# Performance work log

Hardware: AMD Instinct MI355X
Metric: run time of the kernel (lower is better)

## Reference

```python
import jax, jax.numpy as jnp
import numpy as np

B, S, DIM = 4, 2048, 2048
H, KVH, HD = 32, 8, 64
REPEATS = H // KVH
SCALE = HD ** -0.5


def _rope(x, cos, sin):
    # x: (B, S, Hn, HD); cos/sin: (S, HD//2)
    xr = x[..., 0::2]
    xi = x[..., 1::2]
    c = cos[:, None, :]  # (S, 1, HD//2) broadcasts over heads
    s = sin[:, None, :]
    out_r = xr * c - xi * s
    out_i = xr * s + xi * c
    return jnp.stack([out_r, out_i], axis=-1).reshape(x.shape)


def setup_inputs() -> dict:
    key = jax.random.key(0)
    ks = jax.random.split(key, 5)
    x = jax.random.normal(ks[0], (B, S, DIM), dtype=jnp.float32)
    wq = jax.random.normal(ks[1], (H * HD, DIM), dtype=jnp.float32) * 0.02
    wk = jax.random.normal(ks[2], (KVH * HD, DIM), dtype=jnp.float32) * 0.02
    wv = jax.random.normal(ks[3], (KVH * HD, DIM), dtype=jnp.float32) * 0.02
    wo = jax.random.normal(ks[4], (DIM, H * HD), dtype=jnp.float32) * 0.02
    # standard RoPE frequencies: freqs_cis = exp(i * t * theta)
    inv_freq = 1.0 / (10000.0 ** (jnp.arange(0, HD, 2, dtype=jnp.float32) / HD))
    angles = jnp.arange(S, dtype=jnp.float32)[:, None] * inv_freq[None, :]  # (S, HD//2)
    return {
        "x": x, "wq": wq, "wk": wk, "wv": wv, "wo": wo,
        "freqs_cos": jnp.cos(angles), "freqs_sin": jnp.sin(angles),
    }


def reference(x, wq, wk, wv, wo, freqs_cos, freqs_sin):
    b, s, _ = x.shape
    q = (x @ wq.T).reshape(b, s, H, HD)
    k = (x @ wk.T).reshape(b, s, KVH, HD)
    v = (x @ wv.T).reshape(b, s, KVH, HD)
    q = _rope(q, freqs_cos, freqs_sin)
    k = _rope(k, freqs_cos, freqs_sin)
    k_rep = jnp.repeat(k, REPEATS, axis=2)  # (B,S,H,HD)
    v_rep = jnp.repeat(v, REPEATS, axis=2)
    # NOTE: faithful to source - q is NOT transposed to (B,H,S,HD), so the
    # matmul contracts head_dim at each token, producing (B,S,H,H) scores
    # (mixing across heads per position), softmaxed over the last head axis.
    scores = jnp.einsum('bshd,bsed->bshe', q, k_rep) * SCALE  # (B,S,H,H)
    weights = jax.nn.softmax(scores, axis=-1)
    out = jnp.einsum('bshe,bsed->bshd', weights, v_rep)  # (B,S,H,HD)
    out = out.reshape(b, s, H * HD)
    return out @ wo.T
```

## Files before the change

kernel.cpp:

```cpp
#include <hip/hip_runtime.h>

typedef unsigned short u16;
typedef __bf16 bf16x8 __attribute__((ext_vector_type(8)));
typedef float f32x4 __attribute__((ext_vector_type(4)));

#define AS1 __attribute__((address_space(1)))
#define AS3 __attribute__((address_space(3)))

__device__ inline u16 f2bf(float f) {
    union { float f; unsigned u; } c; c.f = f;
    unsigned u = c.u;
    u += 0x7fffu + ((u >> 16) & 1u);
    return (u16)(u >> 16);
}
__device__ inline float bf2f(u16 b) {
    union { unsigned u; float f; } c; c.u = ((unsigned)b) << 16;
    return c.f;
}

__device__ inline void async_cp16(const void* g, void* l) {
    __builtin_amdgcn_global_load_lds((const AS1 void*)g, (AS3 void*)l, 16, 0, 0);
}

__global__ __launch_bounds__(256)
void f32_to_bf16_x8(const float* __restrict__ src, u16* __restrict__ dst) {
    int i = (blockIdx.x * 256 + threadIdx.x) * 8;
    float4 f0 = *(const float4*)(src + i);
    float4 f1 = *(const float4*)(src + i + 4);
    union { u16 h[8]; uint4 v; } o;
    o.h[0] = f2bf(f0.x); o.h[1] = f2bf(f0.y);
    o.h[2] = f2bf(f0.z); o.h[3] = f2bf(f0.w);
    o.h[4] = f2bf(f1.x); o.h[5] = f2bf(f1.y);
    o.h[6] = f2bf(f1.z); o.h[7] = f2bf(f1.w);
    *(uint4*)(dst + i) = o.v;
}

__global__ __launch_bounds__(256)
void conv_weights(const float* __restrict__ wq, const float* __restrict__ wk,
                  const float* __restrict__ wv, const float* __restrict__ wo,
                  u16* __restrict__ wqkv, u16* __restrict__ wo_bf) {
    int i = (blockIdx.x * 256 + threadIdx.x) * 4;
    const float* src;
    u16* dst;
    if (i < 4194304)       { src = wq + i;           dst = wqkv + i; }
    else if (i < 5242880)  { src = wk + (i-4194304); dst = wqkv + i; }
    else if (i < 6291456)  { src = wv + (i-5242880); dst = wqkv + i; }
    else                   { src = wo + (i-6291456); dst = wo_bf + (i-6291456); }
    float4 f = *(const float4*)src;
    union { u16 h[4]; uint2 v; } o;
    o.h[0] = f2bf(f.x); o.h[1] = f2bf(f.y);
    o.h[2] = f2bf(f.z); o.h[3] = f2bf(f.w);
    *(uint2*)dst = o.v;
}

template <bool BF16_OUT>
__global__ __launch_bounds__(256)
void gemm_bt(const u16* __restrict__ A, const u16* __restrict__ B,
             void* __restrict__ Cout, int N, int K) {
    __shared__ u16 ldsA[128 * 64];
    __shared__ u16 ldsB[128 * 64];

    const int tid  = threadIdx.x;
    const int wave = tid >> 6;
    const int lane = tid & 63;
    const int row0 = blockIdx.x * 128;
    const int col0 = blockIdx.y * 128;
    const int waveM = (wave >> 1) * 64;
    const int waveN = (wave & 1) * 64;
    const int lm   = lane & 15;
    const int quad = lane >> 4;

    const int sr  = lane >> 3;
    const int stR = 8 * wave + sr;
    const int stC = ((lane & 7) ^ sr) * 8;
    const u16* gA = A + (size_t)(row0 + stR) * K + stC;
    const u16* gB = B + (size_t)(col0 + stR) * K + stC;
    char* lA = (char*)ldsA + wave * 1024;
    char* lB = (char*)ldsB + wave * 1024;
    const size_t g32K = (size_t)32 * K;

    f32x4 acc[4][4];
#pragma unroll
    for (int i = 0; i < 4; i++)
#pragma unroll
        for (int j = 0; j < 4; j++) acc[i][j] = (f32x4){0.f, 0.f, 0.f, 0.f};

    int aOff[2][4], bOff[2][4];
#pragma unroll
    for (int s = 0; s < 2; s++)
#pragma unroll
        for (int mi = 0; mi < 4; mi++) {
            int rA = waveM + mi * 16 + lm;
            int rB = waveN + mi * 16 + lm;
            int c  = (4 * s + quad) ^ (lm & 7);
            aOff[s][mi] = rA * 128 + c * 16;
            bOff[s][mi] = rB * 128 + c * 16;
        }

    for (int kb = 0; kb < K; kb += 64) {
#pragma unroll
        for (int i = 0; i < 4; i++)
            async_cp16(gA + i * g32K + kb, lA + i * 4096);
#pragma unroll
        for (int i = 0; i < 4; i++)
            async_cp16(gB + i * g32K + kb, lB + i * 4096);
        __syncthreads();

#pragma unroll
        for (int s = 0; s < 2; s++) {
            bf16x8 af[4], bg[4];
#pragma unroll
            for (int mi = 0; mi < 4; mi++)
                af[mi] = *(const bf16x8*)((const char*)ldsA + aOff[s][mi]);
#pragma unroll
            for (int ni = 0; ni < 4; ni++)
                bg[ni] = *(const bf16x8*)((const char*)ldsB + bOff[s][ni]);
#pragma unroll
            for (int mi = 0; mi < 4; mi++)
#pragma unroll
                for (int ni = 0; ni < 4; ni++)
                    acc[mi][ni] = __builtin_amdgcn_mfma_f32_16x16x32_bf16(
                        af[mi], bg[ni], acc[mi][ni], 0, 0, 0);
        }
        __syncthreads();
    }

    const int rbase = row0 + waveM + quad * 4;
    const int cbase = col0 + waveN + lm;
    if (BF16_OUT) {
        u16* C = (u16*)Cout;
#pragma unroll
        for (int mi = 0; mi < 4; mi++)
#pragma unroll
            for (int r = 0; r < 4; r++) {
                size_t ro = (size_t)(rbase + mi * 16 + r) * N;
#pragma unroll
                for (int ni = 0; ni < 4; ni++)
                    C[ro + cbase + ni * 16] = f2bf(acc[mi][ni][r]);
            }
    } else {
        float* C = (float*)Cout;
#pragma unroll
        for (int mi = 0; mi < 4; mi++)
#pragma unroll
            for (int r = 0; r < 4; r++) {
                size_t ro = (size_t)(rbase + mi * 16 + r) * N;
#pragma unroll
                for (int ni = 0; ni < 4; ni++)
                    C[ro + cbase + ni * 16] = acc[mi][ni][r];
            }
    }
}

__global__ __launch_bounds__(256)
void attn_tok(const u16* __restrict__ qkv, u16* __restrict__ out) {
    __shared__ float kvf[1024];
    const int tok = blockIdx.x;
    const int t = threadIdx.x;
    const u16* qrow = qkv + (size_t)tok * 3072;

    {
        uint2 w = *(const uint2*)(qrow + 2048 + t * 4);
        kvf[t * 4 + 0] = bf2f((u16)(w.x & 0xffff));
        kvf[t * 4 + 1] = bf2f((u16)(w.x >> 16));
        kvf[t * 4 + 2] = bf2f((u16)(w.y & 0xffff));
        kvf[t * 4 + 3] = bf2f((u16)(w.y >> 16));
    }
    __syncthreads();

    const int h = t >> 3, j = t & 7;
    float qf[8];
    {
        uint4 w = *(const uint4*)(qrow + h * 64 + j * 8);
        unsigned ws4[4] = {w.x, w.y, w.z, w.w};
#pragma unroll
        for (int i = 0; i < 4; i++) {
            qf[2 * i]     = bf2f((u16)(ws4[i] & 0xffff));
            qf[2 * i + 1] = bf2f((u16)(ws4[i] >> 16));
        }
    }

    float s[8];
#pragma unroll
    for (int g = 0; g < 8; g++) {
        const float* kk = kvf + g * 64 + j * 8;
        float a = 0.f;
#pragma unroll
        for (int d = 0; d < 8; d++) a += qf[d] * kk[d];
        s[g] = a;
    }
#pragma unroll
    for (int g = 0; g < 8; g++) {
        s[g] += __shfl_xor(s[g], 1);
        s[g] += __shfl_xor(s[g], 2);
        s[g] += __shfl_xor(s[g], 4);
    }
    float m = -1e30f;
#pragma unroll
    for (int g = 0; g < 8; g++) { s[g] *= 0.125f; m = fmaxf(m, s[g]); }
    float p[8], l = 0.f;
#pragma unroll
    for (int g = 0; g < 8; g++) { p[g] = __expf(s[g] - m); l += p[g]; }
    float rl = 1.f / l;

    float o[8] = {0, 0, 0, 0, 0, 0, 0, 0};
#pragma unroll
    for (int g = 0; g < 8; g++) {
        float w = p[g] * rl;
        const float* vv = kvf + 512 + g * 64 + j * 8;
#pragma unroll
        for (int d = 0; d < 8; d++) o[d] += w * vv[d];
    }

    unsigned po[4];
#pragma unroll
    for (int i = 0; i < 4; i++)
        po[i] = (unsigned)f2bf(o[2 * i]) | ((unsigned)f2bf(o[2 * i + 1]) << 16);
    uint4 wo_; wo_.x = po[0]; wo_.y = po[1]; wo_.z = po[2]; wo_.w = po[3];
    *(uint4*)(out + (size_t)tok * 2048 + h * 64 + j * 8) = wo_;
}

extern "C" void kernel_launch(void* const* d_in, const int* in_sizes, int n_in,
                              void* d_out, int out_size, void* d_ws, size_t ws_size,
                              hipStream_t stream) {
    const float* x  = (const float*)d_in[0];
    const float* wq = (const float*)d_in[1];
    const float* wk = (const float*)d_in[2];
    const float* wv = (const float*)d_in[3];
    const float* wo = (const float*)d_in[4];

    u16* x_bf  = (u16*)d_ws;
    u16* wqkv  = x_bf  + 16777216;
    u16* wo_bf = wqkv  + 6291456;
    u16* qkv   = wo_bf + 4194304;
    u16* attn  = qkv   + 25165824;

    dim3 blk(256);
    f32_to_bf16_x8<<<8192, blk, 0, stream>>>(x, x_bf);
    conv_weights<<<10240, blk, 0, stream>>>(wq, wk, wv, wo, wqkv, wo_bf);

    gemm_bt<true><<<dim3(64, 24), blk, 0, stream>>>(x_bf, wqkv, qkv, 3072, 2048);

    attn_tok<<<8192, blk, 0, stream>>>(qkv, attn);

    gemm_bt<false><<<dim3(64, 16), blk, 0, stream>>>(attn, wo_bf, (float*)d_out,
                                                     2048, 2048);
}
```

Before: 376.0 us.

## Replace GEMM with 256x256-tile, 8-wave, double-buffered async-LDS pipelined kernel

Both projection GEMMs now use a new kernel with 256x256 output tiles per 512-thread block. It double-buffers 64-wide K slices in 128KB of LDS and issues async global-to-LDS copies for the next slices while MFMAs run on the current ones. Manual waitcnt, barrier and setprio scheduling interleave LDS fragment reads with MFMA phases. This is meant to hide global-load latency and raise data reuse per LDS byte. In exchange it launches far fewer blocks (384 and 256), so it depends on one wave of large blocks keeping all CUs busy, and it adds heavy register pressure.

```diff
diff --git a/kernel.cpp b/kernel.cpp
--- a/kernel.cpp
+++ b/kernel.cpp
@@ -54,83 +54,140 @@
 }
 
 template <bool BF16_OUT>
-__global__ __launch_bounds__(256)
-void gemm_bt(const u16* __restrict__ A, const u16* __restrict__ B,
-             void* __restrict__ Cout, int N, int K) {
-    __shared__ u16 ldsA[128 * 64];
-    __shared__ u16 ldsB[128 * 64];
+__global__ __launch_bounds__(512, 2)
+void gemm_bt8(const u16* __restrict__ A, const u16* __restrict__ B,
+              void* __restrict__ Cout, int N, int K) {
+    __shared__ __align__(16) u16 lds[65536];
+    char* ldsc = (char*)lds;
 
     const int tid  = threadIdx.x;
-    const int wave = tid >> 6;
+    const int w    = tid >> 6;
     const int lane = tid & 63;
-    const int row0 = blockIdx.x * 128;
-    const int col0 = blockIdx.y * 128;
-    const int waveM = (wave >> 1) * 64;
-    const int waveN = (wave & 1) * 64;
-    const int lm   = lane & 15;
-    const int quad = lane >> 4;
+    const int row0 = blockIdx.x * 256;
+    const int col0 = blockIdx.y * 256;
+    const int wm = w >> 2, wn = w & 3;
+    const int lm = lane & 15, quad = lane >> 4;
+
+    const int NT  = K / 64;
+    const int NIT = K / 128;
+    const int K64 = K * 64, K128 = K * 128;
 
     const int sr  = lane >> 3;
-    const int stR = 8 * wave + sr;
     const int stC = ((lane & 7) ^ sr) * 8;
-    const u16* gA = A + (size_t)(row0 + stR) * K + stC;
-    const u16* gB = B + (size_t)(col0 + stR) * K + stC;
-    char* lA = (char*)ldsA + wave * 1024;
-    char* lB = (char*)ldsB + wave * 1024;
-    const size_t g32K = (size_t)32 * K;
-
-    f32x4 acc[4][4];
-#pragma unroll
-    for (int i = 0; i < 4; i++)
+    const u16* pA = A + (size_t)(row0 + w * 8 + sr) * K + stC;
+    const u16* pB = B + (size_t)(col0 + w * 8 + sr) * K + stC;
+    const int stagoff = w * 1024;
+
+    const int cx0   = (quad ^ (lm & 7)) * 16;
+    const int cx1   = cx0 ^ 64;
+    const int aBase = (wm * 128 + lm) * 128;
+    const int bBase = 32768 + (wn * 64 + lm) * 128;
+
+    f32x4 acc[8][4];
+#pragma unroll
+    for (int i = 0; i < 8; i++)
 #pragma unroll
         for (int j = 0; j < 4; j++) acc[i][j] = (f32x4){0.f, 0.f, 0.f, 0.f};
 
-    int aOff[2][4], bOff[2][4];
-#pragma unroll
-    for (int s = 0; s < 2; s++)
-#pragma unroll
-        for (int mi = 0; mi < 4; mi++) {
-            int rA = waveM + mi * 16 + lm;
-            int rB = waveN + mi * 16 + lm;
-            int c  = (4 * s + quad) ^ (lm & 7);
-            aOff[s][mi] = rA * 128 + c * 16;
-            bOff[s][mi] = rB * 128 + c * 16;
-        }
-
-    for (int kb = 0; kb < K; kb += 64) {
-#pragma unroll
-        for (int i = 0; i < 4; i++)
-            async_cp16(gA + i * g32K + kb, lA + i * 4096);
-#pragma unroll
-        for (int i = 0; i < 4; i++)
-            async_cp16(gB + i * g32K + kb, lB + i * 4096);
-        __syncthreads();
-
-#pragma unroll
-        for (int s = 0; s < 2; s++) {
-            bf16x8 af[4], bg[4];
-#pragma unroll
-            for (int mi = 0; mi < 4; mi++)
-                af[mi] = *(const bf16x8*)((const char*)ldsA + aOff[s][mi]);
-#pragma unroll
-            for (int ni = 0; ni < 4; ni++)
-                bg[ni] = *(const bf16x8*)((const char*)ldsB + bOff[s][ni]);
-#pragma unroll
-            for (int mi = 0; mi < 4; mi++)
-#pragma unroll
-                for (int ni = 0; ni < 4; ni++)
-                    acc[mi][ni] = __builtin_amdgcn_mfma_f32_16x16x32_bf16(
-                        af[mi], bg[ni], acc[mi][ni], 0, 0, 0);
-        }
-        __syncthreads();
-    }
-
-    const int rbase = row0 + waveM + quad * 4;
-    const int cbase = col0 + waveN + lm;
+    auto stA = [&](int v, int h) {
+        int kb = (v < NT ? v : NT - 1) * 64;
+        const u16* g = pA + h * K128 + kb;
+        char* d = ldsc + ((v & 1) << 16) + h * 16384 + stagoff;
+        async_cp16(g, d);
+        async_cp16(g + K64, d + 8192);
+    };
+    auto stB = [&](int v, int h) {
+        int kb = (v < NT ? v : NT - 1) * 64;
+        const u16* g = pB + h * K128 + kb;
+        char* d = ldsc + ((v & 1) << 16) + 32768 + h * 16384 + stagoff;
+        async_cp16(g, d);
+        async_cp16(g + K64, d + 8192);
+    };
+
+    stB(0, 0); stB(0, 1); stA(0, 0); stA(0, 1);
+    stB(1, 0); stB(1, 1); stA(1, 0);
+    asm volatile("s_waitcnt vmcnt(6)" ::: "memory");
+    __builtin_amdgcn_s_barrier();
+
+    bf16x8 bg[4][2], afX[2][2], afY[2][2];
+
+#define LDR(off) (*(const bf16x8*)(ldsc + (off)))
+
+#define PHASE_TAIL(MI0, AF)                                                   \
+    __builtin_amdgcn_s_barrier();                                             \
+    asm volatile("s_waitcnt lgkmcnt(0)" ::: "memory");                        \
+    __builtin_amdgcn_sched_barrier(0);                                        \
+    __builtin_amdgcn_s_setprio(1);                                            \
+    _Pragma("unroll")                                                         \
+    for (int s = 0; s < 2; s++)                                               \
+        _Pragma("unroll")                                                     \
+        for (int j = 0; j < 2; j++)                                           \
+            _Pragma("unroll")                                                 \
+            for (int ni = 0; ni < 4; ni++)                                    \
+                acc[(MI0) + j][ni] = __builtin_amdgcn_mfma_f32_16x16x32_bf16( \
+                    AF[j][s], bg[ni][s], acc[(MI0) + j][ni], 0, 0, 0);        \
+    __builtin_amdgcn_s_setprio(0);
+
+#define HALF_ITER(u, BO)                                                      \
+    {                                                                         \
+                                                                      \
+        _Pragma("unroll")                                                     \
+        for (int ni = 0; ni < 4; ni++) {                                      \
+            bg[ni][0] = LDR((BO) + bBase + ni * 2048 + cx0);                  \
+            bg[ni][1] = LDR((BO) + bBase + ni * 2048 + cx1);                  \
+        }                                                                     \
+        _Pragma("unroll")                                                     \
+        for (int j = 0; j < 2; j++) {                                         \
+            afX[j][0] = LDR((BO) + aBase + j * 2048 + cx0);                   \
+            afX[j][1] = LDR((BO) + aBase + j * 2048 + cx1);                   \
+            afY[j][0] = LDR((BO) + aBase + (2 + j) * 2048 + cx0);             \
+            afY[j][1] = LDR((BO) + aBase + (2 + j) * 2048 + cx1);             \
+        }                                                                     \
+        stA((u) + 1, 1);                                                      \
+        asm volatile("s_waitcnt lgkmcnt(8)" ::: "memory");                    \
+        PHASE_TAIL(0, afX)                                                    \
+        __builtin_amdgcn_s_barrier();                                         \
+                                                                      \
+        _Pragma("unroll")                                                     \
+        for (int j = 0; j < 2; j++) {                                         \
+            afX[j][0] = LDR((BO) + aBase + (4 + j) * 2048 + cx0);             \
+            afX[j][1] = LDR((BO) + aBase + (4 + j) * 2048 + cx1);             \
+        }                                                                     \
+        stB((u) + 2, 0);                                                      \
+        PHASE_TAIL(2, afY)                                                    \
+        __builtin_amdgcn_s_barrier();                                         \
+                                                                      \
+        _Pragma("unroll")                                                     \
+        for (int j = 0; j < 2; j++) {                                         \
+            afY[j][0] = LDR((BO) + aBase + (6 + j) * 2048 + cx0);             \
+            afY[j][1] = LDR((BO) + aBase + (6 + j) * 2048 + cx1);             \
+        }                                                                     \
+        stB((u) + 2, 1);                                                      \
+        PHASE_TAIL(4, afX)                                                    \
+        __builtin_amdgcn_s_barrier();                                         \
+                                                                      \
+        stA((u) + 2, 0);                                                      \
+        PHASE_TAIL(6, afY)                                                    \
+        asm volatile("s_waitcnt vmcnt(6)" ::: "memory");                      \
+        __builtin_amdgcn_s_barrier();                                         \
+    }
+
+    for (int it = 0; it < NIT; ++it) {
+        const int t = 2 * it;
+        HALF_ITER(t, 0)
+        HALF_ITER(t + 1, 65536)
+    }
+
+#undef HALF_ITER
+#undef PHASE_TAIL
+#undef LDR
+
+    const int rbase = row0 + wm * 128 + quad * 4;
+    const int cbase = col0 + wn * 64 + lm;
     if (BF16_OUT) {
         u16* C = (u16*)Cout;
 #pragma unroll
-        for (int mi = 0; mi < 4; mi++)
+        for (int mi = 0; mi < 8; mi++)
 #pragma unroll
             for (int r = 0; r < 4; r++) {
                 size_t ro = (size_t)(rbase + mi * 16 + r) * N;
@@ -141,7 +198,7 @@
     } else {
         float* C = (float*)Cout;
 #pragma unroll
-        for (int mi = 0; mi < 4; mi++)
+        for (int mi = 0; mi < 8; mi++)
 #pragma unroll
             for (int r = 0; r < 4; r++) {
                 size_t ro = (size_t)(rbase + mi * 16 + r) * N;
@@ -235,14 +292,13 @@
     u16* qkv   = wo_bf + 4194304;
     u16* attn  = qkv   + 25165824;
 
-    dim3 blk(256);
-    f32_to_bf16_x8<<<8192, blk, 0, stream>>>(x, x_bf);
-    conv_weights<<<10240, blk, 0, stream>>>(wq, wk, wv, wo, wqkv, wo_bf);
-
-    gemm_bt<true><<<dim3(64, 24), blk, 0, stream>>>(x_bf, wqkv, qkv, 3072, 2048);
-
-    attn_tok<<<8192, blk, 0, stream>>>(qkv, attn);
-
-    gemm_bt<false><<<dim3(64, 16), blk, 0, stream>>>(attn, wo_bf, (float*)d_out,
-                                                     2048, 2048);
-}
+    f32_to_bf16_x8<<<8192, dim3(256), 0, stream>>>(x, x_bf);
+    conv_weights<<<10240, dim3(256), 0, stream>>>(wq, wk, wv, wo, wqkv, wo_bf);
+
+    gemm_bt8<true><<<dim3(32, 12), dim3(512), 0, stream>>>(x_bf, wqkv, qkv, 3072, 2048);
+
+    attn_tok<<<8192, dim3(256), 0, stream>>>(qkv, attn);
+
+    gemm_bt8<false><<<dim3(32, 8), dim3(512), 0, stream>>>(attn, wo_bf, (float*)d_out,
+                                                           2048, 2048);
+}
```

Result: faster. 340.0 us (-9.6%).
